# Optimization experiments

Measured on AMD Instinct MI355X. Metric: run time of the kernel, lower is better.

Reference implementation:

```python
import jax, jax.numpy as jnp
import numpy as np

BITS = 8
CLIP_BOUND = 2.0 ** (BITS - 1) - 1.0  # 127 for int8
EPS = 1e-12


def _per_tensor_scale(x):
    # Dynamic per-tensor abs-max calibration (TensorQuantizer.update with
    # calibration over the whole tensor): scale maps abs-max to the clip bound.
    amax = jnp.max(jnp.abs(x))
    return CLIP_BOUND / jnp.maximum(amax, EPS)


def setup_inputs() -> dict:
    key = jax.random.key(0)
    k1, k2 = jax.random.split(key)
    lhs = jax.random.normal(k1, (4096, 4096), dtype=jnp.float32)
    rhs = jax.random.normal(k2, (4096, 4096), dtype=jnp.float32)
    return {"lhs": lhs, "rhs": rhs}


def reference(lhs, rhs):
    # --- calibration (scales are statistics, no gradient flows through them) ---
    ls = _per_tensor_scale(lhs)
    rs = _per_tensor_scale(rhs)

    # --- quantize to int8 grid ---
    ql = jnp.clip(jnp.round(lhs * ls), -CLIP_BOUND, CLIP_BOUND).astype(jnp.int8)
    qr = jnp.clip(jnp.round(rhs * rs), -CLIP_BOUND, CLIP_BOUND).astype(jnp.int8)

    # --- integer dot_general with int32 accumulation (aqt_dot_general core) ---
    dimension_numbers = (((1,), (0,)), ((), ()))
    acc = jax.lax.dot_general(
        ql, qr, dimension_numbers, preferred_element_type=jnp.int32
    )

    # --- dequantize by product of scales ---
    out = acc.astype(jnp.float32) / (ls * rs)
    return out
```

## Files before the change

### kernel.cpp

```cpp
#include <hip/hip_runtime.h>
#include <stdint.h>


#define NROW 4096
#define NELEM (4096 * 4096)

typedef __attribute__((ext_vector_type(4))) int int32x4;
typedef const __attribute__((address_space(1))) int8_t* gptr1_t;
typedef __attribute__((address_space(3))) int8_t* lptr3_t;

__global__ void absmax_both_kernel(const float* __restrict__ lhs,
                                   const float* __restrict__ rhs,
                                   unsigned* __restrict__ amax) {
    __shared__ float red[4];
    const int t = blockIdx.x & 1;
    const float4* x4 = (const float4*)(t ? rhs : lhs);
    const int bid = blockIdx.x >> 1;
    const int stride = (gridDim.x >> 1) * blockDim.x;
    int i = bid * blockDim.x + threadIdx.x;
    float m0 = 0.0f, m1 = 0.0f, m2 = 0.0f, m3 = 0.0f;
    for (; i + 3 * stride < NELEM / 4; i += 4 * stride) {
        float4 a = x4[i];
        float4 b = x4[i + stride];
        float4 c = x4[i + 2 * stride];
        float4 d = x4[i + 3 * stride];
        m0 = fmaxf(m0, fmaxf(fmaxf(fabsf(a.x), fabsf(a.y)),
                             fmaxf(fabsf(a.z), fabsf(a.w))));
        m1 = fmaxf(m1, fmaxf(fmaxf(fabsf(b.x), fabsf(b.y)),
                             fmaxf(fabsf(b.z), fabsf(b.w))));
        m2 = fmaxf(m2, fmaxf(fmaxf(fabsf(c.x), fabsf(c.y)),
                             fmaxf(fabsf(c.z), fabsf(c.w))));
        m3 = fmaxf(m3, fmaxf(fmaxf(fabsf(d.x), fabsf(d.y)),
                             fmaxf(fabsf(d.z), fabsf(d.w))));
    }
    for (; i < NELEM / 4; i += stride) {
        float4 a = x4[i];
        m0 = fmaxf(m0, fmaxf(fmaxf(fabsf(a.x), fabsf(a.y)),
                             fmaxf(fabsf(a.z), fabsf(a.w))));
    }
    float m = fmaxf(fmaxf(m0, m1), fmaxf(m2, m3));
    for (int off = 32; off > 0; off >>= 1)
        m = fmaxf(m, __shfl_down(m, off, 64));
    const int lane = threadIdx.x & 63, wave = threadIdx.x >> 6;
    if (lane == 0) red[wave] = m;
    __syncthreads();
    if (threadIdx.x == 0) {
        float b = fmaxf(fmaxf(red[0], red[1]), fmaxf(red[2], red[3]));
        atomicMax(amax + t, __float_as_uint(b));
    }
}

__device__ __forceinline__ int q8(float v, float s) {
    int r = __float2int_rn(v * s);
    r = r < -127 ? -127 : r;
    r = r > 127 ? 127 : r;
    return r;
}

__global__ void quant_kernel(const float* __restrict__ lhs,
                             const float* __restrict__ rhs,
                             int8_t* __restrict__ qA, int8_t* __restrict__ qT,
                             const unsigned* __restrict__ amax) {
    __shared__ int8_t sm[64][68];
    if (blockIdx.x < 16384) {
        const float s = 127.0f / fmaxf(__uint_as_float(amax[0]), 1e-12f);
        const int i = blockIdx.x * blockDim.x + threadIdx.x;
        float4 v = ((const float4*)lhs)[i];
        int b0 = q8(v.x, s), b1 = q8(v.y, s), b2 = q8(v.z, s), b3 = q8(v.w, s);
        ((int*)qA)[i] = (b0 & 0xff) | ((b1 & 0xff) << 8) | ((b2 & 0xff) << 16)
                      | ((b3 & 0xff) << 24);
    } else {
        const float s = 127.0f / fmaxf(__uint_as_float(amax[1]), 1e-12f);
        const int b = blockIdx.x - 16384;
        const int n0 = (b & 63) * 64, k0 = (b >> 6) * 64;
        const int rl = threadIdx.x >> 4;
        const int nq = threadIdx.x & 15;
        for (int r = 0; r < 4; ++r) {
            const int kl = r * 16 + rl;
            float4 v = *(const float4*)(rhs + (size_t)(k0 + kl) * NROW + n0 + nq * 4);
            sm[nq * 4 + 0][kl] = (int8_t)q8(v.x, s);
            sm[nq * 4 + 1][kl] = (int8_t)q8(v.y, s);
            sm[nq * 4 + 2][kl] = (int8_t)q8(v.z, s);
            sm[nq * 4 + 3][kl] = (int8_t)q8(v.w, s);
        }
        __syncthreads();
        const int nl = threadIdx.x >> 2;
        const int kq = threadIdx.x & 3;
        int4 w;
        w.x = *(const int*)&sm[nl][kq * 16 + 0];
        w.y = *(const int*)&sm[nl][kq * 16 + 4];
        w.z = *(const int*)&sm[nl][kq * 16 + 8];
        w.w = *(const int*)&sm[nl][kq * 16 + 12];
        *(int4*)(qT + (size_t)(n0 + nl) * NROW + k0 + kq * 16) = w;
    }
}

__global__ __launch_bounds__(512, 2) void gemm_i8_kernel(
    const int8_t* __restrict__ qA, const int8_t* __restrict__ qBT,
    float* __restrict__ out, const unsigned* __restrict__ amax) {
    __shared__ __align__(16) int8_t sA[3][256 * 64];
    __shared__ __align__(16) int8_t sB[3][256 * 64];

    const int tid = threadIdx.x;
    const int lane = tid & 63;
    const int wave = tid >> 6;
    const int wm = wave >> 2;
    const int wn = wave & 3;
    const int m0 = blockIdx.y * 256, n0 = blockIdx.x * 256;

    const int r = lane & 15;
    const int q = lane >> 4;

    const int rowA = wm * 128 + r;
    const int aoff = rowA * 64 + ((q + (rowA >> 1)) & 3) * 16;
    const int rowB = wn * 64 + r;
    const int boff = rowB * 64 + ((q + (rowB >> 1)) & 3) * 16;

    const int C0 = tid, C1 = tid + 512;
    const int rS0 = C0 >> 2, G0 = ((C0 & 3) - (rS0 >> 1)) & 3;
    const int rS1 = C1 >> 2, G1 = ((C1 & 3) - (rS1 >> 1)) & 3;
    const gptr1_t pA0 = (gptr1_t)(qA + (size_t)(m0 + rS0) * NROW + G0 * 16);
    const gptr1_t pA1 = (gptr1_t)(qA + (size_t)(m0 + rS1) * NROW + G1 * 16);
    const gptr1_t pB0 = (gptr1_t)(qBT + (size_t)(n0 + rS0) * NROW + G0 * 16);
    const gptr1_t pB1 = (gptr1_t)(qBT + (size_t)(n0 + rS1) * NROW + G1 * 16);
    int8_t* sAf = &sA[0][0];
    int8_t* sBf = &sB[0][0];
    const int d0 = C0 * 16, d1 = C1 * 16;

    int32x4 acc[8][4];
#pragma unroll
    for (int mi = 0; mi < 8; ++mi)
#pragma unroll
        for (int ni = 0; ni < 4; ++ni) acc[mi][ni] = (int32x4)(0);

    auto stage = [&](int buf, int kt) {
        const int kb = kt * 64;
        __builtin_amdgcn_global_load_lds(pA0 + kb, (lptr3_t)(sAf + buf * 16384 + d0), 16, 0, 0);
        __builtin_amdgcn_global_load_lds(pA1 + kb, (lptr3_t)(sAf + buf * 16384 + d1), 16, 0, 0);
        __builtin_amdgcn_global_load_lds(pB0 + kb, (lptr3_t)(sBf + buf * 16384 + d0), 16, 0, 0);
        __builtin_amdgcn_global_load_lds(pB1 + kb, (lptr3_t)(sBf + buf * 16384 + d1), 16, 0, 0);
    };

    auto compute = [&](int cur) {
        const int8_t* a = sAf + cur * 16384;
        const int8_t* b = sBf + cur * 16384;
        int32x4 af[8], bf[4];
#pragma unroll
        for (int mi = 0; mi < 8; ++mi)
            af[mi] = *(const int32x4*)(a + aoff + mi * 1024);
#pragma unroll
        for (int ni = 0; ni < 4; ++ni)
            bf[ni] = *(const int32x4*)(b + boff + ni * 1024);
        __builtin_amdgcn_s_setprio(1);
#pragma unroll
        for (int mi = 0; mi < 8; ++mi)
#pragma unroll
            for (int ni = 0; ni < 4; ++ni)
                acc[mi][ni] = __builtin_amdgcn_mfma_i32_16x16x64_i8(
                    af[mi], bf[ni], acc[mi][ni], 0, 0, 0);
        __builtin_amdgcn_s_setprio(0);
    };

    stage(0, 0);
    stage(1, 1);
    asm volatile("s_waitcnt vmcnt(4)" ::: "memory");
    __builtin_amdgcn_s_barrier();
    __builtin_amdgcn_sched_barrier(0);

    int cur = 0, stg = 2;
#pragma unroll 1
    for (int kt = 0; kt < 62; ++kt) {
        stage(stg, kt + 2);
        compute(cur);
        asm volatile("s_waitcnt vmcnt(4)" ::: "memory");
        __builtin_amdgcn_s_barrier();
        __builtin_amdgcn_sched_barrier(0);
        cur = (cur == 2) ? 0 : cur + 1;
        stg = (stg == 2) ? 0 : stg + 1;
    }
    compute(cur);
    asm volatile("s_waitcnt vmcnt(0)" ::: "memory");
    __builtin_amdgcn_s_barrier();
    __builtin_amdgcn_sched_barrier(0);
    cur = (cur == 2) ? 0 : cur + 1;
    compute(cur);

    const float ls = 127.0f / fmaxf(__uint_as_float(amax[0]), 1e-12f);
    const float rs = 127.0f / fmaxf(__uint_as_float(amax[1]), 1e-12f);
    const float inv = 1.0f / (ls * rs);
#pragma unroll
    for (int mi = 0; mi < 8; ++mi)
#pragma unroll
        for (int ni = 0; ni < 4; ++ni)
#pragma unroll
            for (int reg = 0; reg < 4; ++reg) {
                const int row = m0 + wm * 128 + mi * 16 + q * 4 + reg;
                const int col = n0 + wn * 64 + ni * 16 + r;
                out[(size_t)row * NROW + col] = (float)acc[mi][ni][reg] * inv;
            }
}

extern "C" void kernel_launch(void* const* d_in, const int* in_sizes, int n_in,
                              void* d_out, int out_size, void* d_ws,
                              size_t ws_size, hipStream_t stream) {
    const float* lhs = (const float*)d_in[0];
    const float* rhs = (const float*)d_in[1];
    float* out = (float*)d_out;

    int8_t* qA = (int8_t*)d_ws;
    int8_t* qBT = qA + (size_t)16 * 1024 * 1024;
    unsigned* amax = (unsigned*)(qBT + (size_t)16 * 1024 * 1024);

    hipMemsetAsync(amax, 0, 8, stream);
    absmax_both_kernel<<<2048, 256, 0, stream>>>(lhs, rhs, amax);
    quant_kernel<<<16384 + 4096, 256, 0, stream>>>(lhs, rhs, qA, qBT, amax);
    gemm_i8_kernel<<<dim3(16, 16), 512, 0, stream>>>(qA, qBT, out, amax);
}
```

Before: 156.7 us.

## Interleave GEMM main loop into four barrier-separated MFMA phases with staggered loads

```diff
diff --git a/kernel.cpp b/kernel.cpp
--- a/kernel.cpp
+++ b/kernel.cpp
@@ -95,6 +95,88 @@
     }
 }
 
+template <bool DO_STAGE, int VMN>
+__device__ __forceinline__ void gemm_iter(
+    const int8_t* a, const int8_t* b, int aoff, int boff, int32x4 (&acc)[8][4],
+    gptr1_t pA0, gptr1_t pA1, gptr1_t pB0, gptr1_t pB1,
+    lptr3_t dA0, lptr3_t dA1, lptr3_t dB0, lptr3_t dB1) {
+    int32x4 bf0, bf1, bf2, bf3, a0, a1;
+
+    bf0 = *(const int32x4*)(b + boff);
+    bf1 = *(const int32x4*)(b + boff + 1024);
+    bf2 = *(const int32x4*)(b + boff + 2048);
+    bf3 = *(const int32x4*)(b + boff + 3072);
+    a0 = *(const int32x4*)(a + aoff);
+    a1 = *(const int32x4*)(a + aoff + 1024);
+    if (DO_STAGE) __builtin_amdgcn_global_load_lds(pA0, dA0, 16, 0, 0);
+    __builtin_amdgcn_sched_barrier(0);
+    __builtin_amdgcn_s_barrier();
+    __builtin_amdgcn_s_setprio(1);
+    acc[0][0] = __builtin_amdgcn_mfma_i32_16x16x64_i8(a0, bf0, acc[0][0], 0, 0, 0);
+    acc[0][1] = __builtin_amdgcn_mfma_i32_16x16x64_i8(a0, bf1, acc[0][1], 0, 0, 0);
+    acc[0][2] = __builtin_amdgcn_mfma_i32_16x16x64_i8(a0, bf2, acc[0][2], 0, 0, 0);
+    acc[0][3] = __builtin_amdgcn_mfma_i32_16x16x64_i8(a0, bf3, acc[0][3], 0, 0, 0);
+    acc[1][0] = __builtin_amdgcn_mfma_i32_16x16x64_i8(a1, bf0, acc[1][0], 0, 0, 0);
+    acc[1][1] = __builtin_amdgcn_mfma_i32_16x16x64_i8(a1, bf1, acc[1][1], 0, 0, 0);
+    acc[1][2] = __builtin_amdgcn_mfma_i32_16x16x64_i8(a1, bf2, acc[1][2], 0, 0, 0);
+    acc[1][3] = __builtin_amdgcn_mfma_i32_16x16x64_i8(a1, bf3, acc[1][3], 0, 0, 0);
+    __builtin_amdgcn_s_setprio(0);
+    __builtin_amdgcn_s_barrier();
+
+    a0 = *(const int32x4*)(a + aoff + 2048);
+    a1 = *(const int32x4*)(a + aoff + 3072);
+    if (DO_STAGE) __builtin_amdgcn_global_load_lds(pA1, dA1, 16, 0, 0);
+    __builtin_amdgcn_sched_barrier(0);
+    __builtin_amdgcn_s_barrier();
+    __builtin_amdgcn_s_setprio(1);
+    acc[2][0] = __builtin_amdgcn_mfma_i32_16x16x64_i8(a0, bf0, acc[2][0], 0, 0, 0);
+    acc[2][1] = __builtin_amdgcn_mfma_i32_16x16x64_i8(a0, bf1, acc[2][1], 0, 0, 0);
+    acc[2][2] = __builtin_amdgcn_mfma_i32_16x16x64_i8(a0, bf2, acc[2][2], 0, 0, 0);
+    acc[2][3] = __builtin_amdgcn_mfma_i32_16x16x64_i8(a0, bf3, acc[2][3], 0, 0, 0);
+    acc[3][0] = __builtin_amdgcn_mfma_i32_16x16x64_i8(a1, bf0, acc[3][0], 0, 0, 0);
+    acc[3][1] = __builtin_amdgcn_mfma_i32_16x16x64_i8(a1, bf1, acc[3][1], 0, 0, 0);
+    acc[3][2] = __builtin_amdgcn_mfma_i32_16x16x64_i8(a1, bf2, acc[3][2], 0, 0, 0);
+    acc[3][3] = __builtin_amdgcn_mfma_i32_16x16x64_i8(a1, bf3, acc[3][3], 0, 0, 0);
+    __builtin_amdgcn_s_setprio(0);
+    __builtin_amdgcn_s_barrier();
+
+    a0 = *(const int32x4*)(a + aoff + 4096);
+    a1 = *(const int32x4*)(a + aoff + 5120);
+    if (DO_STAGE) __builtin_amdgcn_global_load_lds(pB0, dB0, 16, 0, 0);
+    __builtin_amdgcn_sched_barrier(0);
+    __builtin_amdgcn_s_barrier();
+    __builtin_amdgcn_s_setprio(1);
+    acc[4][0] = __builtin_amdgcn_mfma_i32_16x16x64_i8(a0, bf0, acc[4][0], 0, 0, 0);
+    acc[4][1] = __builtin_amdgcn_mfma_i32_16x16x64_i8(a0, bf1, acc[4][1], 0, 0, 0);
+    acc[4][2] = __builtin_amdgcn_mfma_i32_16x16x64_i8(a0, bf2, acc[4][2], 0, 0, 0);
+    acc[4][3] = __builtin_amdgcn_mfma_i32_16x16x64_i8(a0, bf3, acc[4][3], 0, 0, 0);
+    acc[5][0] = __builtin_amdgcn_mfma_i32_16x16x64_i8(a1, bf0, acc[5][0], 0, 0, 0);
+    acc[5][1] = __builtin_amdgcn_mfma_i32_16x16x64_i8(a1, bf1, acc[5][1], 0, 0, 0);
+    acc[5][2] = __builtin_amdgcn_mfma_i32_16x16x64_i8(a1, bf2, acc[5][2], 0, 0, 0);
+    acc[5][3] = __builtin_amdgcn_mfma_i32_16x16x64_i8(a1, bf3, acc[5][3], 0, 0, 0);
+    __builtin_amdgcn_s_setprio(0);
+    __builtin_amdgcn_s_barrier();
+
+    a0 = *(const int32x4*)(a + aoff + 6144);
+    a1 = *(const int32x4*)(a + aoff + 7168);
+    if (DO_STAGE) __builtin_amdgcn_global_load_lds(pB1, dB1, 16, 0, 0);
+    if (VMN == 4) asm volatile("s_waitcnt vmcnt(4)" ::: "memory");
+    if (VMN == 0) asm volatile("s_waitcnt vmcnt(0)" ::: "memory");
+    __builtin_amdgcn_sched_barrier(0);
+    __builtin_amdgcn_s_barrier();
+    __builtin_amdgcn_s_setprio(1);
+    acc[6][0] = __builtin_amdgcn_mfma_i32_16x16x64_i8(a0, bf0, acc[6][0], 0, 0, 0);
+    acc[6][1] = __builtin_amdgcn_mfma_i32_16x16x64_i8(a0, bf1, acc[6][1], 0, 0, 0);
+    acc[6][2] = __builtin_amdgcn_mfma_i32_16x16x64_i8(a0, bf2, acc[6][2], 0, 0, 0);
+    acc[6][3] = __builtin_amdgcn_mfma_i32_16x16x64_i8(a0, bf3, acc[6][3], 0, 0, 0);
+    acc[7][0] = __builtin_amdgcn_mfma_i32_16x16x64_i8(a1, bf0, acc[7][0], 0, 0, 0);
+    acc[7][1] = __builtin_amdgcn_mfma_i32_16x16x64_i8(a1, bf1, acc[7][1], 0, 0, 0);
+    acc[7][2] = __builtin_amdgcn_mfma_i32_16x16x64_i8(a1, bf2, acc[7][2], 0, 0, 0);
+    acc[7][3] = __builtin_amdgcn_mfma_i32_16x16x64_i8(a1, bf3, acc[7][3], 0, 0, 0);
+    __builtin_amdgcn_s_setprio(0);
+    __builtin_amdgcn_s_barrier();
+}
+
 __global__ __launch_bounds__(512, 2) void gemm_i8_kernel(
     const int8_t* __restrict__ qA, const int8_t* __restrict__ qBT,
     float* __restrict__ out, const unsigned* __restrict__ amax) {
@@ -133,57 +215,42 @@
 #pragma unroll
         for (int ni = 0; ni < 4; ++ni) acc[mi][ni] = (int32x4)(0);
 
-    auto stage = [&](int buf, int kt) {
-        const int kb = kt * 64;
-        __builtin_amdgcn_global_load_lds(pA0 + kb, (lptr3_t)(sAf + buf * 16384 + d0), 16, 0, 0);
-        __builtin_amdgcn_global_load_lds(pA1 + kb, (lptr3_t)(sAf + buf * 16384 + d1), 16, 0, 0);
-        __builtin_amdgcn_global_load_lds(pB0 + kb, (lptr3_t)(sBf + buf * 16384 + d0), 16, 0, 0);
-        __builtin_amdgcn_global_load_lds(pB1 + kb, (lptr3_t)(sBf + buf * 16384 + d1), 16, 0, 0);
-    };
-
-    auto compute = [&](int cur) {
-        const int8_t* a = sAf + cur * 16384;
-        const int8_t* b = sBf + cur * 16384;
-        int32x4 af[8], bf[4];
-#pragma unroll
-        for (int mi = 0; mi < 8; ++mi)
-            af[mi] = *(const int32x4*)(a + aoff + mi * 1024);
-#pragma unroll
-        for (int ni = 0; ni < 4; ++ni)
-            bf[ni] = *(const int32x4*)(b + boff + ni * 1024);
-        __builtin_amdgcn_s_setprio(1);
-#pragma unroll
-        for (int mi = 0; mi < 8; ++mi)
-#pragma unroll
-            for (int ni = 0; ni < 4; ++ni)
-                acc[mi][ni] = __builtin_amdgcn_mfma_i32_16x16x64_i8(
-                    af[mi], bf[ni], acc[mi][ni], 0, 0, 0);
-        __builtin_amdgcn_s_setprio(0);
-    };
-
-    stage(0, 0);
-    stage(1, 1);
-    asm volatile("s_waitcnt vmcnt(4)" ::: "memory");
-    __builtin_amdgcn_s_barrier();
-    __builtin_amdgcn_sched_barrier(0);
+    {
+        __builtin_amdgcn_global_load_lds(pA0, (lptr3_t)(sAf + d0), 16, 0, 0);
+        __builtin_amdgcn_global_load_lds(pA1, (lptr3_t)(sAf + d1), 16, 0, 0);
+        __builtin_amdgcn_global_load_lds(pB0, (lptr3_t)(sBf + d0), 16, 0, 0);
+        __builtin_amdgcn_global_load_lds(pB1, (lptr3_t)(sBf + d1), 16, 0, 0);
+        __builtin_amdgcn_global_load_lds(pA0 + 64, (lptr3_t)(sAf + 16384 + d0), 16, 0, 0);
+        __builtin_amdgcn_global_load_lds(pA1 + 64, (lptr3_t)(sAf + 16384 + d1), 16, 0, 0);
+        __builtin_amdgcn_global_load_lds(pB0 + 64, (lptr3_t)(sBf + 16384 + d0), 16, 0, 0);
+        __builtin_amdgcn_global_load_lds(pB1 + 64, (lptr3_t)(sBf + 16384 + d1), 16, 0, 0);
+        asm volatile("s_waitcnt vmcnt(4)" ::: "memory");
+        __builtin_amdgcn_sched_barrier(0);
+        __builtin_amdgcn_s_barrier();
+    }
 
     int cur = 0, stg = 2;
 #pragma unroll 1
     for (int kt = 0; kt < 62; ++kt) {
-        stage(stg, kt + 2);
-        compute(cur);
-        asm volatile("s_waitcnt vmcnt(4)" ::: "memory");
-        __builtin_amdgcn_s_barrier();
-        __builtin_amdgcn_sched_barrier(0);
+        const int kb = (kt + 2) * 64;
+        gemm_iter<true, 4>(sAf + cur * 16384, sBf + cur * 16384, aoff, boff,
+                           acc, pA0 + kb, pA1 + kb, pB0 + kb, pB1 + kb,
+                           (lptr3_t)(sAf + stg * 16384 + d0),
+                           (lptr3_t)(sAf + stg * 16384 + d1),
+                           (lptr3_t)(sBf + stg * 16384 + d0),
+                           (lptr3_t)(sBf + stg * 16384 + d1));
         cur = (cur == 2) ? 0 : cur + 1;
         stg = (stg == 2) ? 0 : stg + 1;
     }
-    compute(cur);
-    asm volatile("s_waitcnt vmcnt(0)" ::: "memory");
-    __builtin_amdgcn_s_barrier();
-    __builtin_amdgcn_sched_barrier(0);
+    gemm_iter<false, 0>(sAf + cur * 16384, sBf + cur * 16384, aoff, boff, acc,
+                        pA0, pA1, pB0, pB1, (lptr3_t)(sAf + d0),
+                        (lptr3_t)(sAf + d1), (lptr3_t)(sBf + d0),
+                        (lptr3_t)(sBf + d1));
     cur = (cur == 2) ? 0 : cur + 1;
-    compute(cur);
+    gemm_iter<false, -1>(sAf + cur * 16384, sBf + cur * 16384, aoff, boff, acc,
+                         pA0, pA1, pB0, pB1, (lptr3_t)(sAf + d0),
+                         (lptr3_t)(sAf + d1), (lptr3_t)(sBf + d0),
+                         (lptr3_t)(sBf + d1));
 
     const float ls = 127.0f / fmaxf(__uint_as_float(amax[0]), 1e-12f);
     const float rs = 127.0f / fmaxf(__uint_as_float(amax[1]), 1e-12f);
```

After: 159.3 us. No clear change (+1.6%).

## Double-buffer 128-wide K tiles in int8 GEMM and swizzle block order

Applied to the files above, without the earlier changes.

```diff
diff --git a/kernel.cpp b/kernel.cpp
--- a/kernel.cpp
+++ b/kernel.cpp
@@ -98,34 +98,51 @@
 __global__ __launch_bounds__(512, 2) void gemm_i8_kernel(
     const int8_t* __restrict__ qA, const int8_t* __restrict__ qBT,
     float* __restrict__ out, const unsigned* __restrict__ amax) {
-    __shared__ __align__(16) int8_t sA[3][256 * 64];
-    __shared__ __align__(16) int8_t sB[3][256 * 64];
+    __shared__ __align__(16) int8_t sA[2][256 * 128];
+    __shared__ __align__(16) int8_t sB[2][256 * 128];
 
     const int tid = threadIdx.x;
     const int lane = tid & 63;
     const int wave = tid >> 6;
     const int wm = wave >> 2;
     const int wn = wave & 3;
-    const int m0 = blockIdx.y * 256, n0 = blockIdx.x * 256;
+
+    const int bid = blockIdx.y * 16 + blockIdx.x;
+    const int swz = (bid & 7) * 32 + (bid >> 3);
+    const int m0 = (swz >> 4) * 256, n0 = (swz & 15) * 256;
 
     const int r = lane & 15;
     const int q = lane >> 4;
 
     const int rowA = wm * 128 + r;
-    const int aoff = rowA * 64 + ((q + (rowA >> 1)) & 3) * 16;
+    const int aoff0 = rowA * 128 + (((q + rowA) & 7) << 4);
     const int rowB = wn * 64 + r;
-    const int boff = rowB * 64 + ((q + (rowB >> 1)) & 3) * 16;
-
-    const int C0 = tid, C1 = tid + 512;
-    const int rS0 = C0 >> 2, G0 = ((C0 & 3) - (rS0 >> 1)) & 3;
-    const int rS1 = C1 >> 2, G1 = ((C1 & 3) - (rS1 >> 1)) & 3;
-    const gptr1_t pA0 = (gptr1_t)(qA + (size_t)(m0 + rS0) * NROW + G0 * 16);
-    const gptr1_t pA1 = (gptr1_t)(qA + (size_t)(m0 + rS1) * NROW + G1 * 16);
-    const gptr1_t pB0 = (gptr1_t)(qBT + (size_t)(n0 + rS0) * NROW + G0 * 16);
-    const gptr1_t pB1 = (gptr1_t)(qBT + (size_t)(n0 + rS1) * NROW + G1 * 16);
+    const int boff0 = rowB * 128 + (((q + rowB) & 7) << 4);
+
+    gptr1_t pA[4], pB[4];
+#pragma unroll
+    for (int j = 0; j < 4; ++j) {
+        const int c = tid + j * 512;
+        const int row = c >> 3;
+        const int G = ((c & 7) - row) & 7;
+        pA[j] = (gptr1_t)(qA + (size_t)(m0 + row) * NROW + G * 16);
+        pB[j] = (gptr1_t)(qBT + (size_t)(n0 + row) * NROW + G * 16);
+    }
     int8_t* sAf = &sA[0][0];
     int8_t* sBf = &sB[0][0];
-    const int d0 = C0 * 16, d1 = C1 * 16;
+    const int dst0 = tid * 16;
+
+    auto stage = [&](int slot, int kb) {
+#pragma unroll
+        for (int j = 0; j < 4; ++j) {
+            __builtin_amdgcn_global_load_lds(
+                pA[j] + kb, (lptr3_t)(sAf + slot * 32768 + dst0 + j * 8192),
+                16, 0, 0);
+            __builtin_amdgcn_global_load_lds(
+                pB[j] + kb, (lptr3_t)(sBf + slot * 32768 + dst0 + j * 8192),
+                16, 0, 0);
+        }
+    };
 
     int32x4 acc[8][4];
 #pragma unroll
@@ -133,57 +150,45 @@
 #pragma unroll
         for (int ni = 0; ni < 4; ++ni) acc[mi][ni] = (int32x4)(0);
 
-    auto stage = [&](int buf, int kt) {
-        const int kb = kt * 64;
-        __builtin_amdgcn_global_load_lds(pA0 + kb, (lptr3_t)(sAf + buf * 16384 + d0), 16, 0, 0);
-        __builtin_amdgcn_global_load_lds(pA1 + kb, (lptr3_t)(sAf + buf * 16384 + d1), 16, 0, 0);
-        __builtin_amdgcn_global_load_lds(pB0 + kb, (lptr3_t)(sBf + buf * 16384 + d0), 16, 0, 0);
-        __builtin_amdgcn_global_load_lds(pB1 + kb, (lptr3_t)(sBf + buf * 16384 + d1), 16, 0, 0);
+    auto compute = [&](const int8_t* a, const int8_t* b) {
+#pragma unroll
+        for (int kk = 0; kk < 2; ++kk) {
+            const int ax = aoff0 ^ (kk ? 64 : 0);
+            const int bx = boff0 ^ (kk ? 64 : 0);
+            int32x4 af[8], bf[4];
+#pragma unroll
+            for (int mi = 0; mi < 8; ++mi)
+                af[mi] = *(const int32x4*)(a + ax + mi * 2048);
+#pragma unroll
+            for (int ni = 0; ni < 4; ++ni)
+                bf[ni] = *(const int32x4*)(b + bx + ni * 2048);
+            __builtin_amdgcn_s_setprio(1);
+#pragma unroll
+            for (int mi = 0; mi < 8; ++mi)
+#pragma unroll
+                for (int ni = 0; ni < 4; ++ni)
+                    acc[mi][ni] = __builtin_amdgcn_mfma_i32_16x16x64_i8(
+                        af[mi], bf[ni], acc[mi][ni], 0, 0, 0);
+            __builtin_amdgcn_s_setprio(0);
+        }
     };
 
-    auto compute = [&](int cur) {
-        const int8_t* a = sAf + cur * 16384;
-        const int8_t* b = sBf + cur * 16384;
-        int32x4 af[8], bf[4];
-#pragma unroll
-        for (int mi = 0; mi < 8; ++mi)
-            af[mi] = *(const int32x4*)(a + aoff + mi * 1024);
-#pragma unroll
-        for (int ni = 0; ni < 4; ++ni)
-            bf[ni] = *(const int32x4*)(b + boff + ni * 1024);
-        __builtin_amdgcn_s_setprio(1);
-#pragma unroll
-        for (int mi = 0; mi < 8; ++mi)
-#pragma unroll
-            for (int ni = 0; ni < 4; ++ni)
-                acc[mi][ni] = __builtin_amdgcn_mfma_i32_16x16x64_i8(
-                    af[mi], bf[ni], acc[mi][ni], 0, 0, 0);
-        __builtin_amdgcn_s_setprio(0);
-    };
-
     stage(0, 0);
-    stage(1, 1);
-    asm volatile("s_waitcnt vmcnt(4)" ::: "memory");
+    asm volatile("s_waitcnt vmcnt(0)" ::: "memory");
+    __builtin_amdgcn_sched_barrier(0);
     __builtin_amdgcn_s_barrier();
     __builtin_amdgcn_sched_barrier(0);
 
-    int cur = 0, stg = 2;
 #pragma unroll 1
-    for (int kt = 0; kt < 62; ++kt) {
-        stage(stg, kt + 2);
-        compute(cur);
-        asm volatile("s_waitcnt vmcnt(4)" ::: "memory");
+    for (int w = 0; w < 31; ++w) {
+        stage((w + 1) & 1, (w + 1) * 128);
+        compute(sAf + (w & 1) * 32768, sBf + (w & 1) * 32768);
+        asm volatile("s_waitcnt vmcnt(0)" ::: "memory");
+        __builtin_amdgcn_sched_barrier(0);
         __builtin_amdgcn_s_barrier();
         __builtin_amdgcn_sched_barrier(0);
-        cur = (cur == 2) ? 0 : cur + 1;
-        stg = (stg == 2) ? 0 : stg + 1;
-    }
-    compute(cur);
-    asm volatile("s_waitcnt vmcnt(0)" ::: "memory");
-    __builtin_amdgcn_s_barrier();
-    __builtin_amdgcn_sched_barrier(0);
-    cur = (cur == 2) ? 0 : cur + 1;
-    compute(cur);
+    }
+    compute(sAf + 32768, sBf + 32768);
 
     const float ls = 127.0f / fmaxf(__uint_as_float(amax[0]), 1e-12f);
     const float rs = 127.0f / fmaxf(__uint_as_float(amax[1]), 1e-12f);
```

Result: faster. 139.4 us (-11.1%).
